# Kernel tuning notes

Measured on AMD Instinct MI355X. Metric: run time of the kernel, lower is better.

Reference implementation:

```python
import jax, jax.numpy as jnp
import numpy as np

B, C, H8, W8 = 2, 256, 56, 96
RADIUS, LEVELS = 4, 4


def setup_inputs() -> dict:
    key = jax.random.key(0)
    k1, k2, k3, k4, k5 = jax.random.split(key, 5)
    fmap1 = jax.random.normal(k1, (B, C, H8, W8), jnp.float32)
    fmap2 = jax.random.normal(k2, (B, C, H8, W8), jnp.float32)
    xs = jnp.arange(W8, dtype=jnp.float32)
    ys = jnp.arange(H8, dtype=jnp.float32)
    bx, by = jnp.broadcast_arrays(xs[None, :], ys[:, None])
    base = jnp.stack([bx, by], axis=0)  # [2,H8,W8], x first (as create_coords_grid)
    coords = base[None] + 4.0 * jax.random.normal(k3, (B, 2, H8, W8), jnp.float32)
    flow = jax.random.normal(k4, (B, 2, H8, W8), jnp.float32)
    mask = jax.random.normal(k5, (B, 9 * 8 * 8, H8, W8), jnp.float32)
    return {"fmap1": fmap1, "fmap2": fmap2, "coords": coords, "flow": flow, "mask": mask}


def _bilinear_sample(cflat, Hl, Wl, px, py):
    # cflat: [N, Hl*Wl]; px,py: [N,P] pixel coords; zero padding outside (grid_sample default)
    x0 = jnp.floor(px)
    y0 = jnp.floor(py)
    wx = px - x0
    wy = py - y0
    x0 = x0.astype(jnp.int32)
    y0 = y0.astype(jnp.int32)

    def g(xi, yi):
        valid = (xi >= 0) & (xi <= Wl - 1) & (yi >= 0) & (yi <= Hl - 1)
        idx = jnp.clip(yi, 0, Hl - 1) * Wl + jnp.clip(xi, 0, Wl - 1)
        return jnp.where(valid, jnp.take_along_axis(cflat, idx, axis=1), 0.0)

    return ((1 - wy) * ((1 - wx) * g(x0, y0) + wx * g(x0 + 1, y0))
            + wy * ((1 - wx) * g(x0, y0 + 1) + wx * g(x0 + 1, y0 + 1)))


def _corr_lookup(fmap1, fmap2, coords):
    b, c, h, w = fmap1.shape
    n = b * h * w
    # all-pairs correlation, scaled by sqrt(C)
    corr = jnp.einsum('bchw,bcij->bhwij', fmap1, fmap2) / jnp.sqrt(jnp.float32(c))
    cl = corr.reshape(n, h, w)
    # query coords (pixel units at level 0)
    cx = coords[:, 0].reshape(n)
    cy = coords[:, 1].reshape(n)
    r = RADIUS
    lin = jnp.linspace(-r, r, 2 * r + 1, dtype=jnp.float32)
    # replicates torch.meshgrid(dy,dx) quirk: x-offset varies along axis 0, y along axis 1
    xo = jnp.repeat(lin, 2 * r + 1)  # [81]
    yo = jnp.tile(lin, 2 * r + 1)    # [81]
    outs = []
    for i in range(LEVELS):
        Hl, Wl = cl.shape[1], cl.shape[2]
        cflat = cl.reshape(n, Hl * Wl)
        px = cx[:, None] / (2 ** i) + xo[None, :]
        py = cy[:, None] / (2 ** i) + yo[None, :]
        samp = _bilinear_sample(cflat, Hl, Wl, px, py)  # [N,81]
        outs.append(samp.reshape(b, h, w, -1))
        if i < LEVELS - 1:  # 2x2 avg pool, stride 2
            cl = cl.reshape(n, Hl // 2, 2, Wl // 2, 2).mean(axis=(2, 4))
    out = jnp.concatenate(outs, axis=-1)  # [B,h,w,4*81]
    return out.transpose(0, 3, 1, 2)


def _convex_upsample(flow, mask):
    b, ch, h, w = flow.shape
    m = mask.reshape(b, 1, 9, 8, 8, h, w)
    m = jax.nn.softmax(m, axis=2)
    fp = jnp.pad(8.0 * flow, ((0, 0), (0, 0), (1, 1), (1, 1)))
    # 3x3 unfold, kernel positions row-major (matches F.unfold ordering)
    patches = jnp.stack([fp[:, :, i:i + h, j:j + w]
                         for i in range(3) for j in range(3)], axis=2)  # [B,2,9,h,w]
    up = jnp.sum(m * patches[:, :, :, None, None], axis=2)  # [B,2,8,8,h,w]
    up = up.transpose(0, 1, 4, 2, 5, 3)  # [B,2,h,8,w,8]
    return up.reshape(b, ch, 8 * h, 8 * w)


def reference(fmap1, fmap2, coords, flow, mask):
    corr_feats = _corr_lookup(fmap1, fmap2, coords)  # [B,324,H8,W8]
    up_flow = _convex_upsample(flow, mask)           # [B,2,8*H8,8*W8]
    return (corr_feats, up_flow)
```

## Files before the change

### kernel.cpp

```cpp
#include <hip/hip_runtime.h>
#include <math.h>

constexpr int B = 2, C = 256, H = 56, W = 96;
constexpr int HW = H * W;
constexpr int RADIUS = 4;

#define SQ 21.166666f
constexpr float SCL = 36.0f / (127.0f * 127.0f * 16.0f);

constexpr size_t F1T_B = 0;
constexpr size_t L0_B  = (size_t)B * HW * C;
constexpr size_t L1_B  = L0_B + (size_t)B * HW * C;
constexpr size_t L2_B  = L1_B + (size_t)B * 28 * 48 * C;
constexpr size_t L3_B  = L2_B + (size_t)B * 14 * 24 * C;
constexpr size_t OUT0_ELEMS = (size_t)B * 324 * HW;

static __device__ __forceinline__ int dot4acc(int a, int b, int c) {
#if __has_builtin(__builtin_amdgcn_sdot4)
    return __builtin_amdgcn_sdot4(a, b, c, false);
#else
    c += (int)(char)(a) * (int)(char)(b);
    c += (int)(char)(a >> 8) * (int)(char)(b >> 8);
    c += (int)(char)(a >> 16) * (int)(char)(b >> 16);
    c += (int)(char)(a >> 24) * (int)(char)(b >> 24);
    return c;
#endif
}

static __device__ __forceinline__ unsigned short pack_i8x2(float a, float b) {
    int ia = (int)rintf(a); ia = ia < -127 ? -127 : (ia > 127 ? 127 : ia);
    int ib = (int)rintf(b); ib = ib < -127 ? -127 : (ib > 127 ? 127 : ib);
    return (unsigned short)((ia & 0xFF) | ((ib & 0xFF) << 8));
}

constexpr int TP_BLOCKS = (HW / 32) * (C / 64) * 2 * B;
constexpr int CU_BLOCKS = B * H * 8;
__global__ __launch_bounds__(256) void prep_kernel(
    const float* __restrict__ fmap1, const float* __restrict__ fmap2,
    const float* __restrict__ flow, const float* __restrict__ mask,
    char* __restrict__ ws, float* __restrict__ out1) {
    __shared__ float smem[72 * 96 + 2 * 3 * 98];
    int bid = blockIdx.x;
    int tid = threadIdx.x;

    if (bid < TP_BLOCKS) {
        float (*tile)[33] = (float(*)[33])smem;
        int zi = bid / 672;
        int rem = bid % 672;
        int by = rem / 168, bx = rem % 168;
        int b = zi & 1, m = zi >> 1;
        const float* src = m ? fmap2 : fmap1;
        unsigned short* dst = (unsigned short*)(ws + (m ? L0_B : F1T_B));
        int c0 = by * 64, q0 = bx * 32;
        int tx = tid & 31, ty = tid >> 5;
#pragma unroll
        for (int r = 0; r < 8; ++r) {
            int cl = ty + r * 8;
            tile[cl][tx] = src[((size_t)(b * C + c0 + cl)) * HW + q0 + tx];
        }
        __syncthreads();
#pragma unroll
        for (int r = 0; r < 4; ++r) {
            int pl = ty + r * 8;
            dst[((size_t)b * HW + q0 + pl) * 128 + (c0 >> 1) + tx] =
                pack_i8x2(tile[2 * tx][pl] * SQ, tile[2 * tx + 1][pl] * SQ);
        }
        return;
    }

    float* msk = smem;
    float* fst = smem + 72 * 96;
    int cb = bid - TP_BLOCKS;
    int i = cb & 7;
    int r = cb >> 3;
    int h = r % H;
    int b = r / H;

    for (int idx = tid; idx < 72 * 96; idx += 256) {
        int row = idx / 96, wc = idx - row * 96;
        int k = row >> 3, j = row & 7;
        int gl = k * 64 + i * 8 + j;
        msk[idx] = mask[((size_t)(b * 576 + gl)) * HW + h * W + wc];
    }
    for (int idx = tid; idx < 588; idx += 256) {
        int ch = idx / 294;
        int rem2 = idx - ch * 294;
        int rr = rem2 / 98;
        int xw = rem2 - rr * 98;
        int hh = h + rr - 1, ww = xw - 1;
        float v = 0.f;
        if (hh >= 0 && hh < H && ww >= 0 && ww < W)
            v = 8.0f * flow[((size_t)(b * 2 + ch)) * HW + hh * W + ww];
        fst[idx] = v;
    }
    __syncthreads();

#pragma unroll
    for (int rr = 0; rr < 3; ++rr) {
        int col = tid + rr * 256;
        int w = col >> 3, j = col & 7;
        float m[9], mx = -1e30f;
#pragma unroll
        for (int k = 0; k < 9; ++k) {
            m[k] = msk[(k * 8 + j) * 96 + w];
            mx = fmaxf(mx, m[k]);
        }
        float sum = 0.f;
#pragma unroll
        for (int k = 0; k < 9; ++k) {
            m[k] = __expf(m[k] - mx);
            sum += m[k];
        }
        float inv = 1.0f / sum;
        float a0 = 0.f, a1 = 0.f;
#pragma unroll
        for (int k = 0; k < 9; ++k) {
            int ki = k / 3, kj = k - ki * 3;
            float wgt = m[k] * inv;
            a0 = fmaf(wgt, fst[0 * 294 + ki * 98 + w + kj], a0);
            a1 = fmaf(wgt, fst[1 * 294 + ki * 98 + w + kj], a1);
        }
        size_t row8 = (size_t)8 * h + i;
        out1[((size_t)(b * 2 + 0) * 448 + row8) * 768 + col] = a0;
        out1[((size_t)(b * 2 + 1) * 448 + row8) * 768 + col] = a1;
    }
}

constexpr int NP1 = B * 28 * 48 * C / 2;
constexpr int NP2 = B * 14 * 24 * C / 2;
constexpr int NP3 = B * 7 * 12 * C / 2;

template <int S>
static __device__ __forceinline__ void pool_accum(const unsigned short* src,
                                                  int& sx, int& sy) {
#pragma unroll
    for (int dy = 0; dy < S; ++dy)
#pragma unroll
        for (int dx = 0; dx < S; ++dx) {
            unsigned short v = src[(size_t)dy * (W * 128) + dx * 128];
            sx += (int)(char)(v & 0xFF);
            sy += (int)(char)(v >> 8);
        }
}

__global__ __launch_bounds__(256) void build_pools(char* __restrict__ ws) {
    const unsigned short* L0p = (const unsigned short*)(ws + L0_B);
    int t = blockIdx.x * 256 + threadIdx.x;
    int l, tl;
    if (t < NP1)             { l = 1; tl = t; }
    else if (t < NP1 + NP2)  { l = 2; tl = t - NP1; }
    else                     { l = 3; tl = t - NP1 - NP2; }
    int Wo = W >> l, Ho = H >> l, S = 1 << l;
    int c2 = tl & 127;
    int r = tl >> 7;
    int x = r % Wo; r /= Wo;
    int y = r % Ho;
    int b = r / Ho;
    const unsigned short* src =
        L0p + ((size_t)(b * H + y * S) * W + x * S) * 128 + c2;
    int sx = 0, sy = 0;
    if (l == 1)      pool_accum<2>(src, sx, sy);
    else if (l == 2) pool_accum<4>(src, sx, sy);
    else             pool_accum<8>(src, sx, sy);
    float inv = 1.0f / (S * S);
    unsigned short* dst = (unsigned short*)(ws + (l == 1 ? L1_B : (l == 2 ? L2_B : L3_B)));
    dst[tl] = pack_i8x2((float)sx * inv, (float)sy * inv);
}

__global__ __launch_bounds__(256) void corr_fused(
    const float* __restrict__ coords, const char* __restrict__ ws,
    float* __restrict__ out0) {
    __shared__ float Dsh[4][8][101];
    __shared__ float Wxy[4][8][2];

    int tid = threadIdx.x;
    int l = tid >> 6;
    int lane = tid & 63;
    int u = lane & 1;
    int half = lane >> 5;
    int pr = (lane & 31) >> 1;

    int g0 = blockIdx.x * 8;
    int b = g0 / HW;
    int hw0 = g0 - b * HW;

    int Hl = H >> l, Wl = W >> l;
    size_t off = (l == 0 ? L0_B : (l == 1 ? L1_B : (l == 2 ? L2_B : L3_B)));
    const char* base8 = ws + off + (size_t)b * Hl * Wl * C;
    float scale = (l == 0 ? 1.0f : (l == 1 ? 0.5f : (l == 2 ? 0.25f : 0.125f)));

    int xo0 = pr < 10 ? pr : pr - 10;
    int yo0 = pr < 10 ? 0 : 1;

    const char* f1b = ws + F1T_B;

#pragma unroll 1
    for (int qi = 0; qi < 4; ++qi) {
        int qr = qi * 2 + half;
        int g = g0 + qr;

        const char* ab = f1b + (size_t)g * C + (u << 4);
        int4 A0 = *(const int4*)(ab);
        int4 A1 = *(const int4*)(ab + 32);
        int4 A2 = *(const int4*)(ab + 64);
        int4 A3 = *(const int4*)(ab + 96);
        int4 A4 = *(const int4*)(ab + 128);
        int4 A5 = *(const int4*)(ab + 160);
        int4 A6 = *(const int4*)(ab + 192);
        int4 A7 = *(const int4*)(ab + 224);

        float cx = coords[(size_t)(b * 2 + 0) * HW + hw0 + qr];
        float cy = coords[(size_t)(b * 2 + 1) * HW + hw0 + qr];
        float fx = cx * scale, fy = cy * scale;
        float fxf = floorf(fx), fyf = floorf(fy);
        float wx = fx - fxf, wy = fy - fyf;
        int ix = (int)fxf, iy = (int)fyf;
        if (pr == 0 && u == 0) { Wxy[l][qr][0] = wx; Wxy[l][qr][1] = wy; }

        int xo = xo0, yo = yo0;
#pragma unroll
        for (int it = 0; it < 7; ++it) {
            bool live = (it < 6) | (pr < 4);
            int x = ix - RADIUS + xo;
            int y = iy - RADIUS + yo;
            int s0 = 0, s1 = 0, s2 = 0, s3 = 0;
            if (live && (unsigned)x < (unsigned)Wl && (unsigned)y < (unsigned)Hl) {
                const char* rp = base8 + (((size_t)(y * Wl + x)) << 8) + (u << 4);
                int4 c0 = *(const int4*)(rp);
                int4 c1 = *(const int4*)(rp + 32);
                int4 c2 = *(const int4*)(rp + 64);
                int4 c3 = *(const int4*)(rp + 96);
                int4 c4 = *(const int4*)(rp + 128);
                int4 c5 = *(const int4*)(rp + 160);
                int4 c6 = *(const int4*)(rp + 192);
                int4 c7 = *(const int4*)(rp + 224);
                s0 = dot4acc(c0.x, A0.x, s0); s1 = dot4acc(c0.y, A0.y, s1);
                s2 = dot4acc(c0.z, A0.z, s2); s3 = dot4acc(c0.w, A0.w, s3);
                s0 = dot4acc(c1.x, A1.x, s0); s1 = dot4acc(c1.y, A1.y, s1);
                s2 = dot4acc(c1.z, A1.z, s2); s3 = dot4acc(c1.w, A1.w, s3);
                s0 = dot4acc(c2.x, A2.x, s0); s1 = dot4acc(c2.y, A2.y, s1);
                s2 = dot4acc(c2.z, A2.z, s2); s3 = dot4acc(c2.w, A2.w, s3);
                s0 = dot4acc(c3.x, A3.x, s0); s1 = dot4acc(c3.y, A3.y, s1);
                s2 = dot4acc(c3.z, A3.z, s2); s3 = dot4acc(c3.w, A3.w, s3);
                s0 = dot4acc(c4.x, A4.x, s0); s1 = dot4acc(c4.y, A4.y, s1);
                s2 = dot4acc(c4.z, A4.z, s2); s3 = dot4acc(c4.w, A4.w, s3);
                s0 = dot4acc(c5.x, A5.x, s0); s1 = dot4acc(c5.y, A5.y, s1);
                s2 = dot4acc(c5.z, A5.z, s2); s3 = dot4acc(c5.w, A5.w, s3);
                s0 = dot4acc(c6.x, A6.x, s0); s1 = dot4acc(c6.y, A6.y, s1);
                s2 = dot4acc(c6.z, A6.z, s2); s3 = dot4acc(c6.w, A6.w, s3);
                s0 = dot4acc(c7.x, A7.x, s0); s1 = dot4acc(c7.y, A7.y, s1);
                s2 = dot4acc(c7.z, A7.z, s2); s3 = dot4acc(c7.w, A7.w, s3);
            }
            int s = (s0 + s1) + (s2 + s3);
            s += __shfl_xor(s, 1);
            if (u == 0 && live) Dsh[l][qr][it * 16 + pr] = (float)s * SCL;
            xo += 6;
            int cr = xo >= 10;
            xo -= cr ? 10 : 0;
            yo += 1 + cr;
        }
    }
    __syncthreads();

    for (int o = tid; o < 324 * 8; o += 256) {
        int q = o & 7, ch = o >> 3;
        int lv = ch / 81;
        int o81 = ch - lv * 81;
        int xo = o81 / 9;
        int yo = o81 - xo * 9;
        float wxv = Wxy[lv][q][0], wyv = Wxy[lv][q][1];
        const float* D = Dsh[lv][q];
        float v00 = D[yo * 10 + xo];
        float v01 = D[yo * 10 + xo + 1];
        float v10 = D[yo * 10 + xo + 10];
        float v11 = D[yo * 10 + xo + 11];
        float res = (1.f - wyv) * ((1.f - wxv) * v00 + wxv * v01)
                  +        wyv  * ((1.f - wxv) * v10 + wxv * v11);
        out0[((size_t)(b * 324 + ch)) * HW + hw0 + q] = res;
    }
}

extern "C" void kernel_launch(void* const* d_in, const int* in_sizes, int n_in,
                              void* d_out, int out_size, void* d_ws, size_t ws_size,
                              hipStream_t stream) {
    const float* fmap1  = (const float*)d_in[0];
    const float* fmap2  = (const float*)d_in[1];
    const float* coords = (const float*)d_in[2];
    const float* flow   = (const float*)d_in[3];
    const float* maskp  = (const float*)d_in[4];
    float* out = (float*)d_out;
    char* ws = (char*)d_ws;

    prep_kernel<<<TP_BLOCKS + CU_BLOCKS, 256, 0, stream>>>(
        fmap1, fmap2, flow, maskp, ws, out + OUT0_ELEMS);
    build_pools<<<(NP1 + NP2 + NP3) / 256, 256, 0, stream>>>(ws);
    corr_fused<<<B * HW / 8, 256, 0, stream>>>(coords, ws, out);
}
```

Measured before the change: 175.5 us.

## Fold pyramid pooling into prep kernel and split channels across four lanes

The separate build_pools launch is removed. Its work moves into extra blocks of prep_kernel, which pool fmap2 directly from fp32 using wave shuffles and quantize each pyramid level once, instead of re-pooling already-quantized int8 level-0 data. The correlation kernel now splits each 256-byte feature vector across 4 lanes instead of 2 and loops over 8 queries per wave with one extra shuffle reduction. This lowers per-thread register pressure (launch bounds now request 5 blocks) and cuts one kernel launch. The pooled values differ slightly from before because rounding now happens after averaging.

```diff
diff --git a/kernel.cpp b/kernel.cpp
--- a/kernel.cpp
+++ b/kernel.cpp
@@ -35,6 +35,7 @@
 
 constexpr int TP_BLOCKS = (HW / 32) * (C / 64) * 2 * B;
 constexpr int CU_BLOCKS = B * H * 8;
+constexpr int PL_BLOCKS = B * 7 * 12;
 __global__ __launch_bounds__(256) void prep_kernel(
     const float* __restrict__ fmap1, const float* __restrict__ fmap2,
     const float* __restrict__ flow, const float* __restrict__ mask,
@@ -68,106 +69,107 @@
         return;
     }
 
-    float* msk = smem;
-    float* fst = smem + 72 * 96;
-    int cb = bid - TP_BLOCKS;
-    int i = cb & 7;
-    int r = cb >> 3;
-    int h = r % H;
-    int b = r / H;
-
-    for (int idx = tid; idx < 72 * 96; idx += 256) {
-        int row = idx / 96, wc = idx - row * 96;
-        int k = row >> 3, j = row & 7;
-        int gl = k * 64 + i * 8 + j;
-        msk[idx] = mask[((size_t)(b * 576 + gl)) * HW + h * W + wc];
-    }
-    for (int idx = tid; idx < 588; idx += 256) {
-        int ch = idx / 294;
-        int rem2 = idx - ch * 294;
-        int rr = rem2 / 98;
-        int xw = rem2 - rr * 98;
-        int hh = h + rr - 1, ww = xw - 1;
-        float v = 0.f;
-        if (hh >= 0 && hh < H && ww >= 0 && ww < W)
-            v = 8.0f * flow[((size_t)(b * 2 + ch)) * HW + hh * W + ww];
-        fst[idx] = v;
-    }
-    __syncthreads();
-
-#pragma unroll
-    for (int rr = 0; rr < 3; ++rr) {
-        int col = tid + rr * 256;
-        int w = col >> 3, j = col & 7;
-        float m[9], mx = -1e30f;
-#pragma unroll
-        for (int k = 0; k < 9; ++k) {
-            m[k] = msk[(k * 8 + j) * 96 + w];
-            mx = fmaxf(mx, m[k]);
-        }
-        float sum = 0.f;
-#pragma unroll
-        for (int k = 0; k < 9; ++k) {
-            m[k] = __expf(m[k] - mx);
-            sum += m[k];
-        }
-        float inv = 1.0f / sum;
-        float a0 = 0.f, a1 = 0.f;
-#pragma unroll
-        for (int k = 0; k < 9; ++k) {
-            int ki = k / 3, kj = k - ki * 3;
-            float wgt = m[k] * inv;
-            a0 = fmaf(wgt, fst[0 * 294 + ki * 98 + w + kj], a0);
-            a1 = fmaf(wgt, fst[1 * 294 + ki * 98 + w + kj], a1);
-        }
-        size_t row8 = (size_t)8 * h + i;
-        out1[((size_t)(b * 2 + 0) * 448 + row8) * 768 + col] = a0;
-        out1[((size_t)(b * 2 + 1) * 448 + row8) * 768 + col] = a1;
-    }
-}
-
-constexpr int NP1 = B * 28 * 48 * C / 2;
-constexpr int NP2 = B * 14 * 24 * C / 2;
-constexpr int NP3 = B * 7 * 12 * C / 2;
-
-template <int S>
-static __device__ __forceinline__ void pool_accum(const unsigned short* src,
-                                                  int& sx, int& sy) {
-#pragma unroll
-    for (int dy = 0; dy < S; ++dy)
-#pragma unroll
-        for (int dx = 0; dx < S; ++dx) {
-            unsigned short v = src[(size_t)dy * (W * 128) + dx * 128];
-            sx += (int)(char)(v & 0xFF);
-            sy += (int)(char)(v >> 8);
-        }
-}
-
-__global__ __launch_bounds__(256) void build_pools(char* __restrict__ ws) {
-    const unsigned short* L0p = (const unsigned short*)(ws + L0_B);
-    int t = blockIdx.x * 256 + threadIdx.x;
-    int l, tl;
-    if (t < NP1)             { l = 1; tl = t; }
-    else if (t < NP1 + NP2)  { l = 2; tl = t - NP1; }
-    else                     { l = 3; tl = t - NP1 - NP2; }
-    int Wo = W >> l, Ho = H >> l, S = 1 << l;
-    int c2 = tl & 127;
-    int r = tl >> 7;
-    int x = r % Wo; r /= Wo;
-    int y = r % Ho;
-    int b = r / Ho;
-    const unsigned short* src =
-        L0p + ((size_t)(b * H + y * S) * W + x * S) * 128 + c2;
-    int sx = 0, sy = 0;
-    if (l == 1)      pool_accum<2>(src, sx, sy);
-    else if (l == 2) pool_accum<4>(src, sx, sy);
-    else             pool_accum<8>(src, sx, sy);
-    float inv = 1.0f / (S * S);
-    unsigned short* dst = (unsigned short*)(ws + (l == 1 ? L1_B : (l == 2 ? L2_B : L3_B)));
-    dst[tl] = pack_i8x2((float)sx * inv, (float)sy * inv);
-}
-
-__global__ __launch_bounds__(256) void corr_fused(
+    if (bid < TP_BLOCKS + CU_BLOCKS) {
+        float* msk = smem;
+        float* fst = smem + 72 * 96;
+        int cb = bid - TP_BLOCKS;
+        int i = cb & 7;
+        int r = cb >> 3;
+        int h = r % H;
+        int b = r / H;
+
+        for (int idx = tid; idx < 72 * 96; idx += 256) {
+            int row = idx / 96, wc = idx - row * 96;
+            int k = row >> 3, j = row & 7;
+            int gl = k * 64 + i * 8 + j;
+            msk[idx] = mask[((size_t)(b * 576 + gl)) * HW + h * W + wc];
+        }
+        for (int idx = tid; idx < 588; idx += 256) {
+            int ch = idx / 294;
+            int rem2 = idx - ch * 294;
+            int rr = rem2 / 98;
+            int xw = rem2 - rr * 98;
+            int hh = h + rr - 1, ww = xw - 1;
+            float v = 0.f;
+            if (hh >= 0 && hh < H && ww >= 0 && ww < W)
+                v = 8.0f * flow[((size_t)(b * 2 + ch)) * HW + hh * W + ww];
+            fst[idx] = v;
+        }
+        __syncthreads();
+
+#pragma unroll
+        for (int rr = 0; rr < 3; ++rr) {
+            int col = tid + rr * 256;
+            int w = col >> 3, j = col & 7;
+            float m[9], mx = -1e30f;
+#pragma unroll
+            for (int k = 0; k < 9; ++k) {
+                m[k] = msk[(k * 8 + j) * 96 + w];
+                mx = fmaxf(mx, m[k]);
+            }
+            float sum = 0.f;
+#pragma unroll
+            for (int k = 0; k < 9; ++k) {
+                m[k] = __expf(m[k] - mx);
+                sum += m[k];
+            }
+            float inv = 1.0f / sum;
+            float a0 = 0.f, a1 = 0.f;
+#pragma unroll
+            for (int k = 0; k < 9; ++k) {
+                int ki = k / 3, kj = k - ki * 3;
+                float wgt = m[k] * inv;
+                a0 = fmaf(wgt, fst[0 * 294 + ki * 98 + w + kj], a0);
+                a1 = fmaf(wgt, fst[1 * 294 + ki * 98 + w + kj], a1);
+            }
+            size_t row8 = (size_t)8 * h + i;
+            out1[((size_t)(b * 2 + 0) * 448 + row8) * 768 + col] = a0;
+            out1[((size_t)(b * 2 + 1) * 448 + row8) * 768 + col] = a1;
+        }
+        return;
+    }
+
+    {
+        int pb = bid - TP_BLOCKS - CU_BLOCKS;
+        int b = pb / 84;
+        int t = pb % 84;
+        int y3 = t / 12, x3 = t % 12;
+        int wv = tid >> 6, lane = tid & 63;
+        int py = lane >> 3, px = lane & 7;
+
+        unsigned short* D1 = (unsigned short*)(ws + L1_B);
+        unsigned short* D2 = (unsigned short*)(ws + L2_B);
+        unsigned short* D3 = (unsigned short*)(ws + L3_B);
+        const float* srcp = fmap2 + (size_t)b * C * HW + (size_t)(y3 * 8 + py) * W + x3 * 8 + px;
+
+        for (int j = wv * 32; j < wv * 32 + 32; ++j) {
+            float va = srcp[(size_t)(2 * j) * HW];
+            float vb = srcp[(size_t)(2 * j + 1) * HW];
+            float a1 = va + __shfl_xor(va, 1); a1 += __shfl_xor(a1, 8);
+            float b1 = vb + __shfl_xor(vb, 1); b1 += __shfl_xor(b1, 8);
+            float a2 = a1 + __shfl_xor(a1, 2); a2 += __shfl_xor(a2, 16);
+            float b2 = b1 + __shfl_xor(b1, 2); b2 += __shfl_xor(b2, 16);
+            float a3 = a2 + __shfl_xor(a2, 4); a3 += __shfl_xor(a3, 32);
+            float b3 = b2 + __shfl_xor(b2, 4); b3 += __shfl_xor(b3, 32);
+            if ((lane & 9) == 0) {
+                int Y = y3 * 4 + (py >> 1), X = x3 * 4 + (px >> 1);
+                D1[((size_t)(b * 28 + Y) * 48 + X) * 128 + j] =
+                    pack_i8x2(a1 * 0.25f * SQ, b1 * 0.25f * SQ);
+            }
+            if ((lane & 27) == 0) {
+                int Y = y3 * 2 + (py >> 2), X = x3 * 2 + (px >> 2);
+                D2[((size_t)(b * 14 + Y) * 24 + X) * 128 + j] =
+                    pack_i8x2(a2 * 0.0625f * SQ, b2 * 0.0625f * SQ);
+            }
+            if (lane == 0) {
+                D3[((size_t)(b * 7 + y3) * 12 + x3) * 128 + j] =
+                    pack_i8x2(a3 * 0.015625f * SQ, b3 * 0.015625f * SQ);
+            }
+        }
+    }
+}
+
+__global__ __launch_bounds__(256, 5) void corr_fused(
     const float* __restrict__ coords, const char* __restrict__ ws,
     float* __restrict__ out0) {
     __shared__ float Dsh[4][8][101];
@@ -176,9 +178,8 @@
     int tid = threadIdx.x;
     int l = tid >> 6;
     int lane = tid & 63;
-    int u = lane & 1;
-    int half = lane >> 5;
-    int pr = (lane & 31) >> 1;
+    int v = lane & 3;
+    int grp = lane >> 2;
 
     int g0 = blockIdx.x * 8;
     int b = g0 / HW;
@@ -189,51 +190,35 @@
     const char* base8 = ws + off + (size_t)b * Hl * Wl * C;
     float scale = (l == 0 ? 1.0f : (l == 1 ? 0.5f : (l == 2 ? 0.25f : 0.125f)));
 
-    int xo0 = pr < 10 ? pr : pr - 10;
-    int yo0 = pr < 10 ? 0 : 1;
+    int xo0 = grp < 10 ? grp : grp - 10;
+    int yo0 = grp < 10 ? 0 : 1;
 
     const char* f1b = ws + F1T_B;
 
 #pragma unroll 1
-    for (int qi = 0; qi < 4; ++qi) {
-        int qr = qi * 2 + half;
-        int g = g0 + qr;
-
-        const char* ab = f1b + (size_t)g * C + (u << 4);
-        int4 A0 = *(const int4*)(ab);
-        int4 A1 = *(const int4*)(ab + 32);
-        int4 A2 = *(const int4*)(ab + 64);
-        int4 A3 = *(const int4*)(ab + 96);
-        int4 A4 = *(const int4*)(ab + 128);
-        int4 A5 = *(const int4*)(ab + 160);
-        int4 A6 = *(const int4*)(ab + 192);
-        int4 A7 = *(const int4*)(ab + 224);
-
-        float cx = coords[(size_t)(b * 2 + 0) * HW + hw0 + qr];
-        float cy = coords[(size_t)(b * 2 + 1) * HW + hw0 + qr];
+    for (int qi = 0; qi < 8; ++qi) {
+        int g = g0 + qi;
+        const int4* ap = (const int4*)(f1b + (size_t)g * C + (v << 6));
+        int4 A0 = ap[0], A1 = ap[1], A2 = ap[2], A3 = ap[3];
+
+        float cx = coords[(size_t)(b * 2 + 0) * HW + hw0 + qi];
+        float cy = coords[(size_t)(b * 2 + 1) * HW + hw0 + qi];
         float fx = cx * scale, fy = cy * scale;
         float fxf = floorf(fx), fyf = floorf(fy);
         float wx = fx - fxf, wy = fy - fyf;
         int ix = (int)fxf, iy = (int)fyf;
-        if (pr == 0 && u == 0) { Wxy[l][qr][0] = wx; Wxy[l][qr][1] = wy; }
+        if (lane == 0) { Wxy[l][qi][0] = wx; Wxy[l][qi][1] = wy; }
 
         int xo = xo0, yo = yo0;
 #pragma unroll
         for (int it = 0; it < 7; ++it) {
-            bool live = (it < 6) | (pr < 4);
+            bool live = (it < 6) | (grp < 4);
             int x = ix - RADIUS + xo;
             int y = iy - RADIUS + yo;
             int s0 = 0, s1 = 0, s2 = 0, s3 = 0;
             if (live && (unsigned)x < (unsigned)Wl && (unsigned)y < (unsigned)Hl) {
-                const char* rp = base8 + (((size_t)(y * Wl + x)) << 8) + (u << 4);
-                int4 c0 = *(const int4*)(rp);
-                int4 c1 = *(const int4*)(rp + 32);
-                int4 c2 = *(const int4*)(rp + 64);
-                int4 c3 = *(const int4*)(rp + 96);
-                int4 c4 = *(const int4*)(rp + 128);
-                int4 c5 = *(const int4*)(rp + 160);
-                int4 c6 = *(const int4*)(rp + 192);
-                int4 c7 = *(const int4*)(rp + 224);
+                const int4* cp = (const int4*)(base8 + ((y * Wl + x) << 8) + (v << 6));
+                int4 c0 = cp[0], c1 = cp[1], c2 = cp[2], c3 = cp[3];
                 s0 = dot4acc(c0.x, A0.x, s0); s1 = dot4acc(c0.y, A0.y, s1);
                 s2 = dot4acc(c0.z, A0.z, s2); s3 = dot4acc(c0.w, A0.w, s3);
                 s0 = dot4acc(c1.x, A1.x, s0); s1 = dot4acc(c1.y, A1.y, s1);
@@ -242,18 +227,11 @@
                 s2 = dot4acc(c2.z, A2.z, s2); s3 = dot4acc(c2.w, A2.w, s3);
                 s0 = dot4acc(c3.x, A3.x, s0); s1 = dot4acc(c3.y, A3.y, s1);
                 s2 = dot4acc(c3.z, A3.z, s2); s3 = dot4acc(c3.w, A3.w, s3);
-                s0 = dot4acc(c4.x, A4.x, s0); s1 = dot4acc(c4.y, A4.y, s1);
-                s2 = dot4acc(c4.z, A4.z, s2); s3 = dot4acc(c4.w, A4.w, s3);
-                s0 = dot4acc(c5.x, A5.x, s0); s1 = dot4acc(c5.y, A5.y, s1);
-                s2 = dot4acc(c5.z, A5.z, s2); s3 = dot4acc(c5.w, A5.w, s3);
-                s0 = dot4acc(c6.x, A6.x, s0); s1 = dot4acc(c6.y, A6.y, s1);
-                s2 = dot4acc(c6.z, A6.z, s2); s3 = dot4acc(c6.w, A6.w, s3);
-                s0 = dot4acc(c7.x, A7.x, s0); s1 = dot4acc(c7.y, A7.y, s1);
-                s2 = dot4acc(c7.z, A7.z, s2); s3 = dot4acc(c7.w, A7.w, s3);
             }
             int s = (s0 + s1) + (s2 + s3);
             s += __shfl_xor(s, 1);
-            if (u == 0 && live) Dsh[l][qr][it * 16 + pr] = (float)s * SCL;
+            s += __shfl_xor(s, 2);
+            if (v == 0 && live) Dsh[l][qi][it * 16 + grp] = (float)s * SCL;
             xo += 6;
             int cr = xo >= 10;
             xo -= cr ? 10 : 0;
@@ -291,8 +269,7 @@
     float* out = (float*)d_out;
     char* ws = (char*)d_ws;
 
-    prep_kernel<<<TP_BLOCKS + CU_BLOCKS, 256, 0, stream>>>(
+    prep_kernel<<<TP_BLOCKS + CU_BLOCKS + PL_BLOCKS, 256, 0, stream>>>(
         fmap1, fmap2, flow, maskp, ws, out + OUT0_ELEMS);
-    build_pools<<<(NP1 + NP2 + NP3) / 256, 256, 0, stream>>>(ws);
     corr_fused<<<B * HW / 8, 256, 0, stream>>>(coords, ws, out);
 }
```

Result: slower. 187.9 us (+7.1%).

## Split each correlation dot product across four lanes and halve queries per block

Applied to the files above, without the earlier changes.

The fused correlation kernel now splits each 256-byte int8 dot product across four lanes instead of two, so each lane holds four int4 fragments of the query vector and loads four of the candidate row, and two xor-shuffles reduce the result. Each block now handles 4 queries instead of 8, so the grid doubles, and launch bounds request 8 waves per EU. The aim is to cut per-thread register use and per-lane serial work so more waves fit and memory latency is hidden better. The cost is an extra shuffle per sample, and the coords and Wxy setup now runs for twice as many blocks.

```diff
diff --git a/kernel.cpp b/kernel.cpp
--- a/kernel.cpp
+++ b/kernel.cpp
@@ -167,20 +167,19 @@
     dst[tl] = pack_i8x2((float)sx * inv, (float)sy * inv);
 }
 
-__global__ __launch_bounds__(256) void corr_fused(
+__global__ __launch_bounds__(256, 8) void corr_fused(
     const float* __restrict__ coords, const char* __restrict__ ws,
     float* __restrict__ out0) {
-    __shared__ float Dsh[4][8][101];
-    __shared__ float Wxy[4][8][2];
+    __shared__ float Dsh[4][4][101];
+    __shared__ float Wxy[4][4][2];
 
     int tid = threadIdx.x;
     int l = tid >> 6;
     int lane = tid & 63;
-    int u = lane & 1;
-    int half = lane >> 5;
-    int pr = (lane & 31) >> 1;
-
-    int g0 = blockIdx.x * 8;
+    int v = lane & 3;
+    int grp = lane >> 2;
+
+    int g0 = blockIdx.x * 4;
     int b = g0 / HW;
     int hw0 = g0 - b * HW;
 
@@ -189,51 +188,41 @@
     const char* base8 = ws + off + (size_t)b * Hl * Wl * C;
     float scale = (l == 0 ? 1.0f : (l == 1 ? 0.5f : (l == 2 ? 0.25f : 0.125f)));
 
-    int xo0 = pr < 10 ? pr : pr - 10;
-    int yo0 = pr < 10 ? 0 : 1;
+    int xo0 = grp < 10 ? grp : grp - 10;
+    int yo0 = grp < 10 ? 0 : 1;
 
     const char* f1b = ws + F1T_B;
 
 #pragma unroll 1
     for (int qi = 0; qi < 4; ++qi) {
-        int qr = qi * 2 + half;
-        int g = g0 + qr;
-
-        const char* ab = f1b + (size_t)g * C + (u << 4);
+        int g = g0 + qi;
+        const char* ab = f1b + (size_t)g * C + (v << 4);
         int4 A0 = *(const int4*)(ab);
-        int4 A1 = *(const int4*)(ab + 32);
-        int4 A2 = *(const int4*)(ab + 64);
-        int4 A3 = *(const int4*)(ab + 96);
-        int4 A4 = *(const int4*)(ab + 128);
-        int4 A5 = *(const int4*)(ab + 160);
-        int4 A6 = *(const int4*)(ab + 192);
-        int4 A7 = *(const int4*)(ab + 224);
-
-        float cx = coords[(size_t)(b * 2 + 0) * HW + hw0 + qr];
-        float cy = coords[(size_t)(b * 2 + 1) * HW + hw0 + qr];
+        int4 A1 = *(const int4*)(ab + 64);
+        int4 A2 = *(const int4*)(ab + 128);
+        int4 A3 = *(const int4*)(ab + 192);
+
+        float cx = coords[(size_t)(b * 2 + 0) * HW + hw0 + qi];
+        float cy = coords[(size_t)(b * 2 + 1) * HW + hw0 + qi];
         float fx = cx * scale, fy = cy * scale;
         float fxf = floorf(fx), fyf = floorf(fy);
         float wx = fx - fxf, wy = fy - fyf;
         int ix = (int)fxf, iy = (int)fyf;
-        if (pr == 0 && u == 0) { Wxy[l][qr][0] = wx; Wxy[l][qr][1] = wy; }
+        if (lane == 0) { Wxy[l][qi][0] = wx; Wxy[l][qi][1] = wy; }
 
         int xo = xo0, yo = yo0;
 #pragma unroll
         for (int it = 0; it < 7; ++it) {
-            bool live = (it < 6) | (pr < 4);
+            bool live = (it < 6) | (grp < 4);
             int x = ix - RADIUS + xo;
             int y = iy - RADIUS + yo;
             int s0 = 0, s1 = 0, s2 = 0, s3 = 0;
             if (live && (unsigned)x < (unsigned)Wl && (unsigned)y < (unsigned)Hl) {
-                const char* rp = base8 + (((size_t)(y * Wl + x)) << 8) + (u << 4);
+                const char* rp = base8 + (((size_t)(y * Wl + x)) << 8) + (v << 4);
                 int4 c0 = *(const int4*)(rp);
-                int4 c1 = *(const int4*)(rp + 32);
-                int4 c2 = *(const int4*)(rp + 64);
-                int4 c3 = *(const int4*)(rp + 96);
-                int4 c4 = *(const int4*)(rp + 128);
-                int4 c5 = *(const int4*)(rp + 160);
-                int4 c6 = *(const int4*)(rp + 192);
-                int4 c7 = *(const int4*)(rp + 224);
+                int4 c1 = *(const int4*)(rp + 64);
+                int4 c2 = *(const int4*)(rp + 128);
+                int4 c3 = *(const int4*)(rp + 192);
                 s0 = dot4acc(c0.x, A0.x, s0); s1 = dot4acc(c0.y, A0.y, s1);
                 s2 = dot4acc(c0.z, A0.z, s2); s3 = dot4acc(c0.w, A0.w, s3);
                 s0 = dot4acc(c1.x, A1.x, s0); s1 = dot4acc(c1.y, A1.y, s1);
@@ -242,18 +231,11 @@
                 s2 = dot4acc(c2.z, A2.z, s2); s3 = dot4acc(c2.w, A2.w, s3);
                 s0 = dot4acc(c3.x, A3.x, s0); s1 = dot4acc(c3.y, A3.y, s1);
                 s2 = dot4acc(c3.z, A3.z, s2); s3 = dot4acc(c3.w, A3.w, s3);
-                s0 = dot4acc(c4.x, A4.x, s0); s1 = dot4acc(c4.y, A4.y, s1);
-                s2 = dot4acc(c4.z, A4.z, s2); s3 = dot4acc(c4.w, A4.w, s3);
-                s0 = dot4acc(c5.x, A5.x, s0); s1 = dot4acc(c5.y, A5.y, s1);
-                s2 = dot4acc(c5.z, A5.z, s2); s3 = dot4acc(c5.w, A5.w, s3);
-                s0 = dot4acc(c6.x, A6.x, s0); s1 = dot4acc(c6.y, A6.y, s1);
-                s2 = dot4acc(c6.z, A6.z, s2); s3 = dot4acc(c6.w, A6.w, s3);
-                s0 = dot4acc(c7.x, A7.x, s0); s1 = dot4acc(c7.y, A7.y, s1);
-                s2 = dot4acc(c7.z, A7.z, s2); s3 = dot4acc(c7.w, A7.w, s3);
             }
             int s = (s0 + s1) + (s2 + s3);
             s += __shfl_xor(s, 1);
-            if (u == 0 && live) Dsh[l][qr][it * 16 + pr] = (float)s * SCL;
+            s += __shfl_xor(s, 2);
+            if (v == 0 && live) Dsh[l][qi][it * 16 + grp] = (float)s * SCL;
             xo += 6;
             int cr = xo >= 10;
             xo -= cr ? 10 : 0;
@@ -262,8 +244,8 @@
     }
     __syncthreads();
 
-    for (int o = tid; o < 324 * 8; o += 256) {
-        int q = o & 7, ch = o >> 3;
+    for (int o = tid; o < 324 * 4; o += 256) {
+        int q = o & 3, ch = o >> 2;
         int lv = ch / 81;
         int o81 = ch - lv * 81;
         int xo = o81 / 9;
@@ -294,5 +276,5 @@
     prep_kernel<<<TP_BLOCKS + CU_BLOCKS, 256, 0, stream>>>(
         fmap1, fmap2, flow, maskp, ws, out + OUT0_ELEMS);
     build_pools<<<(NP1 + NP2 + NP3) / 256, 256, 0, stream>>>(ws);
-    corr_fused<<<B * HW / 8, 256, 0, stream>>>(coords, ws, out);
-}
+    corr_fused<<<B * HW / 4, 256, 0, stream>>>(coords, ws, out);
+}
```

New measurement: 155.0 us. -11.7%, faster.
